# Kernel tuning notes

Measured on AMD Instinct MI355X. Metric: run time of the kernel, lower is better.

Reference implementation:

```python
import jax, jax.numpy as jnp
import numpy as np

NUM_R = 725
NUM_T = 180
EPS = 1e-6


def _hough(img):
    """Discrete Hough transform: params[r, t] = sum of img along line
    x*cos(theta_t) + y*sin(theta_t) = rho_r.
    Gather form: sweep along the longer axis of the line (x-sweep when
    |sin|>=|cos|, else y-sweep) so every line is sampled densely.
    """
    W, H = img.shape  # assume square (W == H) so both sweeps share length
    diag = jnp.sqrt(jnp.asarray(W * W + H * H, dtype=img.dtype))
    thetas = jnp.arange(NUM_T, dtype=img.dtype) * (jnp.pi / NUM_T)      # [T]
    rhos = jnp.linspace(-diag, diag, NUM_R, dtype=img.dtype)            # [R]
    cos_t = jnp.cos(thetas)                                             # [T]
    sin_t = jnp.sin(thetas)                                             # [T]
    n = jnp.arange(W)                                                   # sweep coord [N]
    nf = n.astype(img.dtype)

    rho_b = rhos[:, None, None]          # [R,1,1]
    cos_b = cos_t[None, :, None]         # [1,T,1]
    sin_b = sin_t[None, :, None]
    n_b = nf[None, None, :]              # [1,1,N]

    # --- x-sweep: x = n, y = (rho - x*cos) / sin ---
    sin_safe = jnp.where(jnp.abs(sin_b) < EPS, jnp.asarray(1.0, img.dtype), sin_b)
    y_f = (rho_b - n_b * cos_b) / sin_safe
    y_i = jnp.round(y_f).astype(jnp.int32)                              # [R,T,N]
    valid_x = (y_i >= 0) & (y_i < H)
    vals_x = jnp.where(valid_x,
                       img[n[None, None, :], jnp.clip(y_i, 0, H - 1)],
                       jnp.asarray(0.0, img.dtype))

    # --- y-sweep: y = n, x = (rho - y*sin) / cos ---
    cos_safe = jnp.where(jnp.abs(cos_b) < EPS, jnp.asarray(1.0, img.dtype), cos_b)
    x_f = (rho_b - n_b * sin_b) / cos_safe
    x_i = jnp.round(x_f).astype(jnp.int32)
    valid_y = (x_i >= 0) & (x_i < W)
    vals_y = jnp.where(valid_y,
                       img[jnp.clip(x_i, 0, W - 1), n[None, None, :]],
                       jnp.asarray(0.0, img.dtype))

    use_x = (jnp.abs(sin_t) >= jnp.abs(cos_t))[None, :, None]           # [1,T,1]
    vals = jnp.where(use_x, vals_x, vals_y)
    return jnp.sum(vals, axis=-1)                                        # [R,T]


def setup_inputs() -> dict:
    key = jax.random.key(0)
    img = jax.random.uniform(key, (512, 512), dtype=jnp.float32)
    return {"img": img}


def reference(img):
    return _hough(img)
```

## Files before the change

kernel.cpp:

```cpp
#include <hip/hip_runtime.h>
#include <math.h>

#define W 512
#define H 512
#define NUM_R 725
#define NUM_T 180
#define RCHUNK 32
#define NCHUNK (H / RCHUNK)
#define RPAD 768

#define WS_FLOATS ((size_t)W * H + (size_t)NCHUNK * NUM_T * RPAD)

__global__ __launch_bounds__(256) void transpose_k(const float* __restrict__ in,
                                                   float* __restrict__ out) {
    __shared__ float tile[32][33];
    const int bx = blockIdx.x * 32, by = blockIdx.y * 32;
    const int tx = threadIdx.x, ty = threadIdx.y;
#pragma unroll
    for (int j = 0; j < 32; j += 8)
        tile[ty + j][tx] = in[(size_t)(by + ty + j) * W + (bx + tx)];
    __syncthreads();
#pragma unroll
    for (int j = 0; j < 32; j += 8)
        out[(size_t)(bx + ty + j) * H + (by + tx)] = tile[tx][ty + j];
}

template <int P>
__device__ __forceinline__ void run16(const float4* __restrict__ rp, int rstep,
                                      long long u, long long lqa,
                                      long long L1, long long L2, long long L3,
                                      unsigned B, float* __restrict__ racc_w) {
#pragma unroll
    for (int per = 0; per < 16 / P; ++per) {
        float a0 = 0.f, a1 = 0.f, a2 = 0.f, a3 = 0.f;
        long long u0 = 0, u1 = 0, u2 = 0, u3 = 0;
#pragma unroll
        for (int p = 0; p < P; ++p) {
            const float4 v = rp[(per * P + p) * rstep];
            u0 = u; u1 = u + L1; u2 = u + L2; u3 = u + L3;
            a0 += ((unsigned)u0 <= B) ? v.x : 0.f;
            a1 += ((unsigned)u1 <= B) ? v.y : 0.f;
            a2 += ((unsigned)u2 <= B) ? v.z : 0.f;
            a3 += ((unsigned)u3 <= B) ? v.w : 0.f;
            if (p < P - 1) u += lqa;
        }
        racc_w[(int)(u0 >> 32)] += a0;
        racc_w[(int)(u1 >> 32)] += a1;
        racc_w[(int)(u2 >> 32)] += a2;
        racc_w[(int)(u3 >> 32)] += a3;
        u += lqa;
    }
}

__global__ __launch_bounds__(256) void hough_scatter_k(const float* __restrict__ img,
                                                       const float* __restrict__ imgT,
                                                       float* __restrict__ partial) {
    const int t   = blockIdx.x;
    const int n0  = blockIdx.y * RCHUNK;
    const int tid = threadIdx.x;
    const int wave = tid >> 6;

    __shared__ float racc[4 * RPAD];

    {
        float4* z = (float4*)racc;
#pragma unroll
        for (int k = 0; k < 3; ++k)
            z[tid + 256 * k] = make_float4(0.f, 0.f, 0.f, 0.f);
    }
    __syncthreads();

    const double theta = (double)t * (M_PI / 180.0);
    const double s = sin(theta);
    const double c = cos(theta);
    const bool use_x = fabs(s) >= fabs(c);
    const double diag = sqrt(524288.0);
    const double step = (2.0 * diag) / 724.0;
    const double inv_step = 1.0 / step;

    const double lane_co = (use_x ? s : c) * inv_step;
    const double loop_co = (use_x ? c : s) * inv_step;
    const double dstep   = diag * inv_step;
    const double lane_a  = fabs(lane_co);
    const double loop_a  = fabs(loop_co);

    const double SC = 4294967296.0;
    const long long laneq = (long long)rint(lane_co * SC);
    const long long lqa   = llabs((long long)rint(loop_co * SC));
    const long long L1 = laneq, L2 = 2 * laneq, L3 = 3 * laneq;
    const unsigned hwq = (unsigned)(lane_a * 0.5 * SC);
    const unsigned B = 2u * hwq;

    int P = 2;
    if      (lane_a + 15.0 * loop_a < 0.98) P = 16;
    else if (lane_a +  7.0 * loop_a < 0.98) P = 8;
    else if (lane_a +  3.0 * loop_a < 0.98) P = 4;

    const int h  = tid >> 7;
    const int c0 = (tid & 127) * 4;
    const int rbase = n0 + 16 * h;
    const bool neg = (loop_co < 0.0);
    const int rstart = neg ? rbase + 15 : rbase;
    const int rstep  = neg ? -(W / 4) : (W / 4);

    long long u = (long long)rint(((double)rstart * loop_co +
                                   (double)c0 * lane_co + dstep) * SC)
                + (long long)hwq;

    float* racc_w = racc + wave * RPAD;
    const float* __restrict__ base = use_x ? img : imgT;
    const float4* rp = (const float4*)base + (size_t)rstart * (W / 4) + (tid & 127);

    switch (P) {
        case 16: run16<16>(rp, rstep, u, lqa, L1, L2, L3, B, racc_w); break;
        case 8:  run16<8> (rp, rstep, u, lqa, L1, L2, L3, B, racc_w); break;
        case 4:  run16<4> (rp, rstep, u, lqa, L1, L2, L3, B, racc_w); break;
        default: run16<2> (rp, rstep, u, lqa, L1, L2, L3, B, racc_w); break;
    }

    __syncthreads();

    float* dst = partial + ((size_t)blockIdx.y * NUM_T + t) * RPAD;
#pragma unroll
    for (int k = 0; k < 3; ++k) {
        const int r = tid + 256 * k;
        dst[r] = racc[r] + racc[RPAD + r] + racc[2 * RPAD + r] + racc[3 * RPAD + r];
    }
}

__global__ __launch_bounds__(256) void reduce_k(const float* __restrict__ partial,
                                                float* __restrict__ out) {
    const int t = blockIdx.x;
    const int tid = threadIdx.x;
#pragma unroll
    for (int k = 0; k < 3; ++k) {
        const int r = tid + 256 * k;
        if (r < NUM_R) {
            float acc = 0.f;
#pragma unroll
            for (int ch = 0; ch < NCHUNK; ++ch)
                acc += partial[((size_t)ch * NUM_T + t) * RPAD + r];
            out[(size_t)r * NUM_T + t] = acc;
        }
    }
}

__global__ __launch_bounds__(256) void hough_gather_k(const float* __restrict__ img,
                                                      float* __restrict__ out) {
    const int t = blockIdx.x;
    const int r = blockIdx.y * 256 + threadIdx.x;
    const int rc = (r < NUM_R) ? r : (NUM_R - 1);

    const double theta = (double)t * (M_PI / 180.0);
    const double s = sin(theta);
    const double c = cos(theta);
    const bool use_x = fabs(s) >= fabs(c);
    double dd = use_x ? s : c;
    if (fabs(dd) < 1e-6) dd = 1.0;
    const double a = use_x ? c : s;
    const double inv = 1.0 / dd;
    const double nk2 = -(a * inv);
    const double diag = sqrt(524288.0);
    const double step = (2.0 * diag) / 724.0;
    double rho = (double)rc * step - diag;
    if (rc == NUM_R - 1) rho = diag;

    const double SCALE = 1099511627776.0;
    const long long NK2q = (long long)rint(nk2 * SCALE);
    long long Y = (long long)rint(rho * inv * SCALE) + (1ll << 39);

    float acc = 0.f;
    if (use_x) {
#pragma unroll 8
        for (int n = 0; n < W; ++n) {
            const int y = (int)(Y >> 40);
            Y += NK2q;
            const float v = img[n * W + min(max(y, 0), W - 1)];
            acc += ((unsigned)y < (unsigned)W) ? v : 0.f;
        }
    } else {
#pragma unroll 4
        for (int n = 0; n < W; ++n) {
            const int y = (int)(Y >> 40);
            Y += NK2q;
            const float v = img[min(max(y, 0), W - 1) * W + n];
            acc += ((unsigned)y < (unsigned)W) ? v : 0.f;
        }
    }
    if (r < NUM_R) out[(size_t)r * NUM_T + t] = acc;
}

extern "C" void kernel_launch(void* const* d_in, const int* in_sizes, int n_in,
                              void* d_out, int out_size, void* d_ws, size_t ws_size,
                              hipStream_t stream) {
    const float* img = (const float*)d_in[0];
    float* out = (float*)d_out;

    if (ws_size >= WS_FLOATS * sizeof(float)) {
        float* imgT    = (float*)d_ws;
        float* partial = (float*)d_ws + (size_t)W * H;

        transpose_k<<<dim3(16, 16), dim3(32, 8), 0, stream>>>(img, imgT);
        hough_scatter_k<<<dim3(NUM_T, NCHUNK), dim3(256), 0, stream>>>(img, imgT, partial);
        reduce_k<<<dim3(NUM_T), dim3(256), 0, stream>>>(partial, out);
    } else {
        hough_gather_k<<<dim3(NUM_T, (NUM_R + 255) / 256), dim3(256), 0, stream>>>(img, out);
    }
}
```

Baseline: 73.02 us.

## Process two angles per scatter block to reuse loaded image rows

Each scatter block now handles a pair of adjacent thetas, so a loaded float4 of image rows feeds the accumulators of both angles when they use the same sweep orientation. This halves the grid, doubles the shared-memory accumulator and raises register pressure. The run length P becomes the minimum of the two angles' values, and the negative-slope iteration is reworked to walk forward and choose the bin index from the start or end of the run. The aim is to cut global loads and per-block setup, at the cost of lower occupancy and possibly shorter runs with more atomic-free LDS adds.

```diff
diff --git a/kernel.cpp b/kernel.cpp
--- a/kernel.cpp
+++ b/kernel.cpp
@@ -25,51 +25,60 @@
         out[(size_t)(bx + ty + j) * H + (by + tx)] = tile[tx][ty + j];
 }
 
-template <int P>
-__device__ __forceinline__ void run16(const float4* __restrict__ rp, int rstep,
-                                      long long u, long long lqa,
-                                      long long L1, long long L2, long long L3,
-                                      unsigned B, float* __restrict__ racc_w) {
+template <int P, bool MIXED>
+__device__ __forceinline__ void run16(const float4* __restrict__ rpA,
+                                      const float4* __restrict__ rpB,
+                                      long long uA, long long uB,
+                                      long long lqA, long long lqB,
+                                      long long A1, long long A2, long long A3,
+                                      long long B1, long long B2, long long B3,
+                                      unsigned BA, unsigned BB,
+                                      float* __restrict__ raccA,
+                                      float* __restrict__ raccB) {
 #pragma unroll
     for (int per = 0; per < 16 / P; ++per) {
-        float a0 = 0.f, a1 = 0.f, a2 = 0.f, a3 = 0.f;
-        long long u0 = 0, u1 = 0, u2 = 0, u3 = 0;
+        const long long ufA = uA, ufB = uB;
+        float aA0 = 0.f, aA1 = 0.f, aA2 = 0.f, aA3 = 0.f;
+        float aB0 = 0.f, aB1 = 0.f, aB2 = 0.f, aB3 = 0.f;
 #pragma unroll
         for (int p = 0; p < P; ++p) {
-            const float4 v = rp[(per * P + p) * rstep];
-            u0 = u; u1 = u + L1; u2 = u + L2; u3 = u + L3;
-            a0 += ((unsigned)u0 <= B) ? v.x : 0.f;
-            a1 += ((unsigned)u1 <= B) ? v.y : 0.f;
-            a2 += ((unsigned)u2 <= B) ? v.z : 0.f;
-            a3 += ((unsigned)u3 <= B) ? v.w : 0.f;
-            if (p < P - 1) u += lqa;
-        }
-        racc_w[(int)(u0 >> 32)] += a0;
-        racc_w[(int)(u1 >> 32)] += a1;
-        racc_w[(int)(u2 >> 32)] += a2;
-        racc_w[(int)(u3 >> 32)] += a3;
-        u += lqa;
-    }
-}
-
-__global__ __launch_bounds__(256) void hough_scatter_k(const float* __restrict__ img,
-                                                       const float* __restrict__ imgT,
-                                                       float* __restrict__ partial) {
-    const int t   = blockIdx.x;
-    const int n0  = blockIdx.y * RCHUNK;
-    const int tid = threadIdx.x;
-    const int wave = tid >> 6;
-
-    __shared__ float racc[4 * RPAD];
-
-    {
-        float4* z = (float4*)racc;
-#pragma unroll
-        for (int k = 0; k < 3; ++k)
-            z[tid + 256 * k] = make_float4(0.f, 0.f, 0.f, 0.f);
-    }
-    __syncthreads();
-
+            const int ro = (per * P + p) * (W / 4);
+            const float4 vA = rpA[ro];
+            const float4 vB = MIXED ? rpB[ro] : vA;
+            aA0 += ((unsigned)(uA)      <= BA) ? vA.x : 0.f;
+            aA1 += ((unsigned)(uA + A1) <= BA) ? vA.y : 0.f;
+            aA2 += ((unsigned)(uA + A2) <= BA) ? vA.z : 0.f;
+            aA3 += ((unsigned)(uA + A3) <= BA) ? vA.w : 0.f;
+            aB0 += ((unsigned)(uB)      <= BB) ? vB.x : 0.f;
+            aB1 += ((unsigned)(uB + B1) <= BB) ? vB.y : 0.f;
+            aB2 += ((unsigned)(uB + B2) <= BB) ? vB.z : 0.f;
+            aB3 += ((unsigned)(uB + B3) <= BB) ? vB.w : 0.f;
+            if (p < P - 1) { uA += lqA; uB += lqB; }
+        }
+        const long long sA = (lqA >= 0) ? uA : ufA;
+        const long long sB = (lqB >= 0) ? uB : ufB;
+        raccA[(int)((sA)      >> 32)] += aA0;
+        raccA[(int)((sA + A1) >> 32)] += aA1;
+        raccA[(int)((sA + A2) >> 32)] += aA2;
+        raccA[(int)((sA + A3) >> 32)] += aA3;
+        raccB[(int)((sB)      >> 32)] += aB0;
+        raccB[(int)((sB + B1) >> 32)] += aB1;
+        raccB[(int)((sB + B2) >> 32)] += aB2;
+        raccB[(int)((sB + B3) >> 32)] += aB3;
+        uA += lqA; uB += lqB;
+    }
+}
+
+struct ThetaP {
+    long long u0;
+    long long lq;
+    long long L1, L2, L3;
+    unsigned B;
+    int P;
+    bool use_x;
+};
+
+__device__ __forceinline__ ThetaP theta_params(int t, int rbase, int c0) {
     const double theta = (double)t * (M_PI / 180.0);
     const double s = sin(theta);
     const double c = cos(theta);
@@ -77,54 +86,97 @@
     const double diag = sqrt(524288.0);
     const double step = (2.0 * diag) / 724.0;
     const double inv_step = 1.0 / step;
-
     const double lane_co = (use_x ? s : c) * inv_step;
     const double loop_co = (use_x ? c : s) * inv_step;
     const double dstep   = diag * inv_step;
     const double lane_a  = fabs(lane_co);
     const double loop_a  = fabs(loop_co);
-
     const double SC = 4294967296.0;
+
+    ThetaP tp;
+    tp.use_x = use_x;
     const long long laneq = (long long)rint(lane_co * SC);
-    const long long lqa   = llabs((long long)rint(loop_co * SC));
-    const long long L1 = laneq, L2 = 2 * laneq, L3 = 3 * laneq;
+    tp.lq = (long long)rint(loop_co * SC);
+    tp.L1 = laneq; tp.L2 = 2 * laneq; tp.L3 = 3 * laneq;
     const unsigned hwq = (unsigned)(lane_a * 0.5 * SC);
-    const unsigned B = 2u * hwq;
-
-    int P = 2;
-    if      (lane_a + 15.0 * loop_a < 0.98) P = 16;
-    else if (lane_a +  7.0 * loop_a < 0.98) P = 8;
-    else if (lane_a +  3.0 * loop_a < 0.98) P = 4;
+    tp.B = 2u * hwq;
+    tp.P = 2;
+    if      (lane_a + 15.0 * loop_a < 0.98) tp.P = 16;
+    else if (lane_a +  7.0 * loop_a < 0.98) tp.P = 8;
+    else if (lane_a +  3.0 * loop_a < 0.98) tp.P = 4;
+    tp.u0 = (long long)rint(((double)rbase * loop_co +
+                             (double)c0 * lane_co + dstep) * SC)
+          + (long long)hwq;
+    return tp;
+}
+
+__global__ __launch_bounds__(256) void hough_scatter_k(const float* __restrict__ img,
+                                                       const float* __restrict__ imgT,
+                                                       float* __restrict__ partial) {
+    const int tA  = 2 * blockIdx.x;
+    const int tB  = tA + 1;
+    const int n0  = blockIdx.y * RCHUNK;
+    const int tid = threadIdx.x;
+    const int wave = tid >> 6;
+
+    __shared__ float racc[4 * 2 * RPAD];
+
+    {
+        float4* z = (float4*)racc;
+#pragma unroll
+        for (int k = 0; k < 6; ++k)
+            z[tid + 256 * k] = make_float4(0.f, 0.f, 0.f, 0.f);
+    }
+    __syncthreads();
 
     const int h  = tid >> 7;
     const int c0 = (tid & 127) * 4;
     const int rbase = n0 + 16 * h;
-    const bool neg = (loop_co < 0.0);
-    const int rstart = neg ? rbase + 15 : rbase;
-    const int rstep  = neg ? -(W / 4) : (W / 4);
-
-    long long u = (long long)rint(((double)rstart * loop_co +
-                                   (double)c0 * lane_co + dstep) * SC)
-                + (long long)hwq;
-
-    float* racc_w = racc + wave * RPAD;
-    const float* __restrict__ base = use_x ? img : imgT;
-    const float4* rp = (const float4*)base + (size_t)rstart * (W / 4) + (tid & 127);
-
-    switch (P) {
-        case 16: run16<16>(rp, rstep, u, lqa, L1, L2, L3, B, racc_w); break;
-        case 8:  run16<8> (rp, rstep, u, lqa, L1, L2, L3, B, racc_w); break;
-        case 4:  run16<4> (rp, rstep, u, lqa, L1, L2, L3, B, racc_w); break;
-        default: run16<2> (rp, rstep, u, lqa, L1, L2, L3, B, racc_w); break;
-    }
+
+    const ThetaP pa = theta_params(tA, rbase, c0);
+    const ThetaP pb = theta_params(tB, rbase, c0);
+
+    float* raccA = racc + (wave * 2 + 0) * RPAD;
+    float* raccB = racc + (wave * 2 + 1) * RPAD;
+
+    const float4* rpA = (const float4*)(pa.use_x ? img : imgT)
+                      + (size_t)rbase * (W / 4) + (tid & 127);
+    const float4* rpB = (const float4*)(pb.use_x ? img : imgT)
+                      + (size_t)rbase * (W / 4) + (tid & 127);
+
+    const int P = min(pa.P, pb.P);
+    const bool mixed = (pa.use_x != pb.use_x);
+
+#define RUN(PP, MM) run16<PP, MM>(rpA, rpB, pa.u0, pb.u0, pa.lq, pb.lq, \
+        pa.L1, pa.L2, pa.L3, pb.L1, pb.L2, pb.L3, pa.B, pb.B, raccA, raccB)
+    if (!mixed) {
+        switch (P) {
+            case 16: RUN(16, false); break;
+            case 8:  RUN(8,  false); break;
+            case 4:  RUN(4,  false); break;
+            default: RUN(2,  false); break;
+        }
+    } else {
+        switch (P) {
+            case 16: RUN(16, true); break;
+            case 8:  RUN(8,  true); break;
+            case 4:  RUN(4,  true); break;
+            default: RUN(2,  true); break;
+        }
+    }
+#undef RUN
 
     __syncthreads();
 
-    float* dst = partial + ((size_t)blockIdx.y * NUM_T + t) * RPAD;
+    float* dstA = partial + ((size_t)blockIdx.y * NUM_T + tA) * RPAD;
+    float* dstB = partial + ((size_t)blockIdx.y * NUM_T + tB) * RPAD;
 #pragma unroll
     for (int k = 0; k < 3; ++k) {
         const int r = tid + 256 * k;
-        dst[r] = racc[r] + racc[RPAD + r] + racc[2 * RPAD + r] + racc[3 * RPAD + r];
+        dstA[r] = racc[0 * RPAD + r] + racc[2 * RPAD + r]
+                + racc[4 * RPAD + r] + racc[6 * RPAD + r];
+        dstB[r] = racc[1 * RPAD + r] + racc[3 * RPAD + r]
+                + racc[5 * RPAD + r] + racc[7 * RPAD + r];
     }
 }
 
@@ -201,7 +253,7 @@
         float* partial = (float*)d_ws + (size_t)W * H;
 
         transpose_k<<<dim3(16, 16), dim3(32, 8), 0, stream>>>(img, imgT);
-        hough_scatter_k<<<dim3(NUM_T, NCHUNK), dim3(256), 0, stream>>>(img, imgT, partial);
+        hough_scatter_k<<<dim3(NUM_T / 2, NCHUNK), dim3(256), 0, stream>>>(img, imgT, partial);
         reduce_k<<<dim3(NUM_T), dim3(256), 0, stream>>>(partial, out);
     } else {
         hough_gather_k<<<dim3(NUM_T, (NUM_R + 255) / 256), dim3(256), 0, stream>>>(img, out);
```

Result: slower. 75.47 us (+3.4%).
